# Performance work log

Measured on AMD Instinct MI355X. Metric: run time of the kernel, lower is better.

The kernel has to match this reference:

```python
import jax, jax.numpy as jnp
import numpy as np

K = 3  # number of propagation hops in SGConv


def setup_inputs() -> dict:
    key = jax.random.key(0)
    k1, k2, k3, k4 = jax.random.split(key, 4)
    N, E, F_in, F_out = 100000, 1600000, 32, 64
    x = jax.random.normal(k1, (N, F_in), dtype=jnp.float32)
    edge_index = jax.random.randint(k2, (2, E), 0, N, dtype=jnp.int64)
    # Linear(in_channels, hidden_channels) params, torch layout: W [out, in], b [out]
    lim = 1.0 / np.sqrt(F_in)
    W = jax.random.uniform(k3, (F_out, F_in), minval=-lim, maxval=lim, dtype=jnp.float32)
    b = jax.random.uniform(k4, (F_out,), minval=-lim, maxval=lim, dtype=jnp.float32)
    return {"x": x, "edge_index": edge_index, "W": W, "b": b}


def reference(x, edge_index, W, b):
    N = x.shape[0]
    # gcn_norm: add self-loops with weight 1, symmetric normalization
    loop = jnp.arange(N, dtype=edge_index.dtype)
    src = jnp.concatenate([edge_index[0], loop])  # [E+N] message sources (x_j)
    dst = jnp.concatenate([edge_index[1], loop])  # [E+N] aggregation targets
    ones = jnp.ones(src.shape[0], dtype=x.dtype)
    deg = jax.ops.segment_sum(ones, dst, num_segments=N)  # in-degree incl. self-loop
    dinv = jnp.where(deg > 0, jax.lax.rsqrt(deg), 0.0)
    norm = dinv[src] * dinv[dst]  # [E+N]
    # K hops of normalized sparse propagation: x <- \hat{A} x
    h = x
    for _ in range(K):
        h = jax.ops.segment_sum(norm[:, None] * h[src], dst, num_segments=N)
    # final linear transform
    return h @ W.T + b
```

## Files before the change

### kernel.cpp

```cpp
#include <hip/hip_runtime.h>


#define F_IN 32
#define F_OUT 64
#define SB_SHIFT 13
#define NSB_MAX 16
#define SUB_SHIFT 8
#define SUB (1 << SUB_SHIFT)
#define SPS 32
#define EPB1 2048
#define EPB2 4096
#define SCAP 147456
#define SUBCAP 6144
#define BPS (SCAP / EPB2)

typedef float f4 __attribute__((ext_vector_type(4)));
typedef float f8 __attribute__((ext_vector_type(8)));
typedef _Float16 h4 __attribute__((ext_vector_type(4)));
typedef _Float16 h8 __attribute__((ext_vector_type(8)));
typedef int i2 __attribute__((ext_vector_type(2)));

__global__ __launch_bounds__(256) void k_bin1(const int* __restrict__ ei,
                                              int* __restrict__ scur,
                                              unsigned* __restrict__ b1, int E) {
    __shared__ unsigned stage[EPB1];
    __shared__ unsigned char bidl[EPB1];
    __shared__ int h4w[4][NSB_MAX];
    __shared__ int f4w[4][NSB_MAX];
    __shared__ int lscanx[NSB_MAX], lbase[NSB_MAX];
    unsigned rec[EPB1 / 256];
    int      bk[EPB1 / 256];
    int tid = threadIdx.x;
    int wv = tid >> 6;
    int base = blockIdx.x * EPB1;
    int cnt = E - base; if (cnt > EPB1) cnt = EPB1;

    if (tid < 64) { h4w[tid >> 4][tid & 15] = 0; }
    __syncthreads();
#pragma unroll
    for (int k = 0; k < EPB1 / 256; ++k) {
        int i = base + k * 256 + tid;
        bk[k] = -1;
        if (i < E) {
            unsigned s = (unsigned)ei[i];
            unsigned d = (unsigned)ei[E + i];
            int b = d >> SB_SHIFT;
            rec[k] = (s << SB_SHIFT) | (d & ((1u << SB_SHIFT) - 1));
            bk[k] = b;
            atomicAdd(&h4w[wv][b], 1);
        }
    }
    __syncthreads();
    if (tid < 16) {
        int t0 = h4w[0][tid], t1 = h4w[1][tid], t2 = h4w[2][tid], t3 = h4w[3][tid];
        int tot = t0 + t1 + t2 + t3;
        int inc = tot;
#pragma unroll
        for (int off = 1; off < 16; off <<= 1) {
            int t = __shfl_up(inc, off);
            if (tid >= off) inc += t;
        }
        int excl = inc - tot;
        lscanx[tid] = excl;
        lbase[tid] = tot ? atomicAdd(&scur[tid], tot) : 0;
        f4w[0][tid] = excl;
        f4w[1][tid] = excl + t0;
        f4w[2][tid] = excl + t0 + t1;
        f4w[3][tid] = excl + t0 + t1 + t2;
    }
    __syncthreads();
#pragma unroll
    for (int k = 0; k < EPB1 / 256; ++k) {
        if (bk[k] >= 0) {
            int loc = atomicAdd(&f4w[wv][bk[k]], 1);
            stage[loc] = rec[k];
            bidl[loc] = (unsigned char)bk[k];
        }
    }
    __syncthreads();
    for (int k = 0; k < EPB1 / 256; ++k) {
        int idx = k * 256 + tid;
        if (idx < cnt) {
            int b = bidl[idx];
            b1[(size_t)b * SCAP + lbase[b] + (idx - lscanx[b])] = stage[idx];
        }
    }
}

__global__ __launch_bounds__(256) void k_bin2(const unsigned* __restrict__ b1,
                                              const int* __restrict__ scur,
                                              int* __restrict__ subcur,
                                              unsigned* __restrict__ b2) {
    int sb = blockIdx.x / BPS;
    int base = (blockIdx.x % BPS) * EPB2;
    int count = scur[sb];
    if (base >= count) return;
    int cnt = count - base; if (cnt > EPB2) cnt = EPB2;
    const unsigned* src = b1 + (size_t)sb * SCAP + base;

    __shared__ unsigned stage[EPB2];
    __shared__ unsigned char bidl[EPB2];
    __shared__ int h4w[4][SPS];
    __shared__ int f4w[4][SPS];
    __shared__ int lscanx[SPS], lbase[SPS];
    unsigned rec[EPB2 / 256];
    int tid = threadIdx.x;
    int wv = tid >> 6;
    if (tid < 128) h4w[tid >> 5][tid & 31] = 0;
    __syncthreads();
#pragma unroll
    for (int k = 0; k < EPB2 / 256; ++k) {
        int i = k * 256 + tid;
        rec[k] = 0xFFFFFFFFu;
        if (i < cnt) {
            unsigned r = src[i];
            rec[k] = r;
            atomicAdd(&h4w[wv][(r >> SUB_SHIFT) & (SPS - 1)], 1);
        }
    }
    __syncthreads();
    if (tid < 32) {
        int t0 = h4w[0][tid], t1 = h4w[1][tid], t2 = h4w[2][tid], t3 = h4w[3][tid];
        int tot = t0 + t1 + t2 + t3;
        int inc = tot;
#pragma unroll
        for (int off = 1; off < 32; off <<= 1) {
            int t = __shfl_up(inc, off);
            if (tid >= off) inc += t;
        }
        int excl = inc - tot;
        lscanx[tid] = excl;
        lbase[tid] = tot ? atomicAdd(&subcur[sb * SPS + tid], tot) : 0;
        f4w[0][tid] = excl;
        f4w[1][tid] = excl + t0;
        f4w[2][tid] = excl + t0 + t1;
        f4w[3][tid] = excl + t0 + t1 + t2;
    }
    __syncthreads();
#pragma unroll
    for (int k = 0; k < EPB2 / 256; ++k) {
        if (rec[k] != 0xFFFFFFFFu) {
            int b = (rec[k] >> SUB_SHIFT) & (SPS - 1);
            int loc = atomicAdd(&f4w[wv][b], 1);
            stage[loc] = rec[k];
            bidl[loc] = (unsigned char)b;
        }
    }
    __syncthreads();
    for (int k = 0; k < EPB2 / 256; ++k) {
        int idx = k * 256 + tid;
        if (idx < cnt) {
            unsigned r = stage[idx];
            int b = bidl[idx];
            unsigned packed = ((r >> SB_SHIFT) << SUB_SHIFT) | (r & (SUB - 1));
            b2[(size_t)(sb * SPS + b) * SUBCAP + lbase[b] + (idx - lscanx[b])] = packed;
        }
    }
}

__global__ __launch_bounds__(256) void k_fill3(const unsigned* __restrict__ b2,
                                               const int* __restrict__ subcur,
                                               const f4* __restrict__ x,
                                               float* __restrict__ dinv,
                                               i2* __restrict__ rp2,
                                               int* __restrict__ col,
                                               h8* __restrict__ g0, int N) {
    __shared__ unsigned stage[SUBCAP];
    __shared__ int h[SUB];
    __shared__ float dl[SUB];
    __shared__ int wsum[4];
    int tid = threadIdx.x;
    int g = blockIdx.x;
    int count = subcur[g];
    int sbase = g * SUBCAP;
    int n0 = g << SUB_SHIFT;

    h[tid] = 0;
    for (int e = tid; e < count; e += 256) stage[e] = b2[(size_t)sbase + e];
    __syncthreads();
    for (int e = tid; e < count; e += 256) atomicAdd(&h[stage[e] & (SUB - 1)], 1);
    __syncthreads();

    int deg = h[tid];
    int lane = tid & 63, wid = tid >> 6;
    int inc = deg;
#pragma unroll
    for (int off = 1; off < 64; off <<= 1) {
        int t = __shfl_up(inc, off);
        if (lane >= off) inc += t;
    }
    if (lane == 63) wsum[wid] = inc;
    __syncthreads();
    if (wid == 0) {
        int v = (lane < 4) ? wsum[lane] : 0;
#pragma unroll
        for (int off = 1; off < 4; off <<= 1) {
            int t = __shfl_up(v, off);
            if (lane >= off) v += t;
        }
        if (lane < 4) wsum[lane] = v;
    }
    __syncthreads();
    int incl = inc + (wid ? wsum[wid - 1] : 0);
    int excl = incl - deg;

    int node = n0 + tid;
    float di = rsqrtf(1.0f + (float)deg);
    dl[tid] = di;
    if (node < N) {
        dinv[node] = di;
        rp2[node] = (i2){sbase + excl, sbase + incl};
    }
    h[tid] = excl;
    __syncthreads();

    for (int e = tid; e < count; e += 256) {
        unsigned r = stage[e];
        int slot = sbase + atomicAdd(&h[r & (SUB - 1)], 1);
        col[slot] = (int)(r >> SUB_SHIFT);
    }

    for (int idx = tid; idx < SUB * 4; idx += 256) {
        int nl = idx >> 2;
        int q = idx & 3;
        int node2 = n0 + nl;
        if (node2 < N) {
            int gi = node2 * 8 + q * 2;
            f4 vlo = dl[nl] * x[gi];
            f4 vhi = dl[nl] * x[gi + 1];
            f8 v = __builtin_shufflevector(vlo, vhi, 0, 1, 2, 3, 4, 5, 6, 7);
            g0[(size_t)node2 * 4 + q] = __builtin_convertvector(v, h8);
        }
    }
}

__global__ __launch_bounds__(256) void k_hop_gather(const i2* __restrict__ rp2,
                                                    const int* __restrict__ col,
                                                    const float* __restrict__ dinv,
                                                    const h8* __restrict__ gin,
                                                    h8* __restrict__ gout, int N) {
    int t = blockIdx.x * blockDim.x + threadIdx.x;
    int n = t >> 2;
    if (n >= N) return;
    int q = t & 3;
    i2 r2 = rp2[n];
    int e0 = r2.x, e1 = r2.y;
    f8 a0 = __builtin_convertvector(gin[(size_t)n * 4 + q], f8);
    f8 a1 = {0.f, 0.f, 0.f, 0.f, 0.f, 0.f, 0.f, 0.f};
    int e = e0;
    for (; e + 3 < e1; e += 4) {
        int s0 = col[e], s1 = col[e + 1], s2 = col[e + 2], s3 = col[e + 3];
        h8 h0 = gin[(size_t)s0 * 4 + q];
        h8 h1 = gin[(size_t)s1 * 4 + q];
        h8 h2 = gin[(size_t)s2 * 4 + q];
        h8 h3 = gin[(size_t)s3 * 4 + q];
        a0 += __builtin_convertvector(h0, f8);
        a1 += __builtin_convertvector(h1, f8);
        a0 += __builtin_convertvector(h2, f8);
        a1 += __builtin_convertvector(h3, f8);
    }
    for (; e < e1; ++e) a0 += __builtin_convertvector(gin[(size_t)col[e] * 4 + q], f8);
    float di = dinv[n];
    float sc = di * di;
    f8 r = sc * (a0 + a1);
    gout[(size_t)n * 4 + q] = __builtin_convertvector(r, h8);
}

__global__ __launch_bounds__(256) void k_hop3_linear(const i2* __restrict__ rp2,
                                                     const int* __restrict__ col,
                                                     const float* __restrict__ dinv,
                                                     const h8* __restrict__ gin,
                                                     const float* __restrict__ W,
                                                     const float* __restrict__ bias,
                                                     float* __restrict__ out, int N) {
    __shared__ float Wl[F_OUT][F_IN + 1];
    __shared__ float hl[64][F_IN + 1];
    int tid = threadIdx.x;
    for (int idx = tid; idx < F_OUT * F_IN; idx += 256)
        Wl[idx >> 5][idx & 31] = W[idx];

    int nl = tid >> 2;
    int q = tid & 3;
    int nbase = blockIdx.x * 64;
    int n = nbase + nl;
    if (n < N) {
        i2 r2 = rp2[n];
        int e0 = r2.x, e1 = r2.y;
        f8 a0 = __builtin_convertvector(gin[(size_t)n * 4 + q], f8);
        f8 a1 = {0.f, 0.f, 0.f, 0.f, 0.f, 0.f, 0.f, 0.f};
        int e = e0;
        for (; e + 3 < e1; e += 4) {
            int s0 = col[e], s1 = col[e + 1], s2 = col[e + 2], s3 = col[e + 3];
            h8 h0 = gin[(size_t)s0 * 4 + q];
            h8 h1 = gin[(size_t)s1 * 4 + q];
            h8 h2 = gin[(size_t)s2 * 4 + q];
            h8 h3 = gin[(size_t)s3 * 4 + q];
            a0 += __builtin_convertvector(h0, f8);
            a1 += __builtin_convertvector(h1, f8);
            a0 += __builtin_convertvector(h2, f8);
            a1 += __builtin_convertvector(h3, f8);
        }
        for (; e < e1; ++e) a0 += __builtin_convertvector(gin[(size_t)col[e] * 4 + q], f8);
        float di = dinv[n];
        f8 r = di * (a0 + a1);
#pragma unroll
        for (int i = 0; i < 8; ++i) hl[nl][q * 8 + i] = r[i];
    }
    __syncthreads();
    int o = tid & 63;
    float wreg[F_IN];
#pragma unroll
    for (int f = 0; f < F_IN; ++f) wreg[f] = Wl[o][f];
    float bv = bias[o];
    int nchunk = tid >> 6;
#pragma unroll
    for (int p = 0; p < 16; ++p) {
        int nloc = p * 4 + nchunk;
        int nn = nbase + nloc;
        if (nn < N) {
            float acc = bv;
#pragma unroll
            for (int f = 0; f < F_IN; ++f) acc += hl[nloc][f] * wreg[f];
            out[(size_t)nn * F_OUT + o] = acc;
        }
    }
}

extern "C" void kernel_launch(void* const* d_in, const int* in_sizes, int n_in,
                              void* d_out, int out_size, void* d_ws, size_t ws_size,
                              hipStream_t stream) {
    const float* x  = (const float*)d_in[0];
    const int*   ei = (const int*)d_in[1];
    const float* W  = (const float*)d_in[2];
    const float* b  = (const float*)d_in[3];
    float* out = (float*)d_out;

    const int N = in_sizes[0] / F_IN;
    const int E = in_sizes[1] / 2;
    const int NSB  = (N + (1 << SB_SHIFT) - 1) >> SB_SHIFT;
    const int NSUB = (N + SUB - 1) >> SUB_SHIFT;

    int* scur   = (int*)d_ws;
    int* subcur = scur + NSB_MAX;
    i2*  rp2    = (i2*)(subcur + NSB_MAX * SPS);
    float* dinv = (float*)(rp2 + N);
    unsigned* b1 = (unsigned*)(((uintptr_t)(dinv + N) + 255) & ~(uintptr_t)255);
    unsigned* b2 = b1 + (size_t)NSB_MAX * SCAP;
    int* col     = (int*)(b2 + (size_t)NSB_MAX * SPS * SUBCAP);
    _Float16* hA = (_Float16*)(((uintptr_t)(col + (size_t)NSB_MAX * SPS * SUBCAP) + 255)
                               & ~(uintptr_t)255);
    _Float16* hB = hA + (size_t)N * F_IN;

    const int B = 256;
    dim3 blk(B);

    hipMemsetAsync(scur, 0, (NSB_MAX + NSB_MAX * SPS) * sizeof(int), stream);

    k_bin1<<<dim3((E + EPB1 - 1) / EPB1), blk, 0, stream>>>(ei, scur, b1, E);
    k_bin2<<<dim3(NSB * BPS), blk, 0, stream>>>(b1, scur, subcur, b2);

    k_fill3<<<dim3(NSUB), blk, 0, stream>>>(b2, subcur, (const f4*)x,
                                            dinv, rp2, col, (h8*)hA, N);

    dim3 gHop(((size_t)N * 4 + B - 1) / B);
    k_hop_gather<<<gHop, blk, 0, stream>>>(rp2, col, dinv, (const h8*)hA, (h8*)hB, N);
    k_hop_gather<<<gHop, blk, 0, stream>>>(rp2, col, dinv, (const h8*)hB, (h8*)hA, N);

    k_hop3_linear<<<dim3((N + 63) / 64), blk, 0, stream>>>(rp2, col, dinv,
                                                           (const h8*)hA, W, b, out, N);
}
```

Before: 200.6 us.

## Fuse three propagation hops and linear into one cooperative kernel

Replaces the two per-hop gather launches and the final hop-plus-linear launch with a single cooperative kernel. The hops are separated by grid-wide syncs, and each thread loads its row pointers and degree scale only once. The aim is to remove inter-kernel launch gaps and tail drain between hops. The cost is that all blocks must be resident at once, checked through an occupancy query that assumes 256 compute units, and each grid sync has its own overhead. If the cooperative launch is not possible, the code falls back to the original three launches.

```diff
diff --git a/kernel.cpp b/kernel.cpp
--- a/kernel.cpp
+++ b/kernel.cpp
@@ -1,4 +1,7 @@
 #include <hip/hip_runtime.h>
+#include <hip/hip_cooperative_groups.h>
+
+namespace cg = cooperative_groups;
 
 
 #define F_IN 32
@@ -16,7 +19,6 @@
 
 typedef float f4 __attribute__((ext_vector_type(4)));
 typedef float f8 __attribute__((ext_vector_type(8)));
-typedef _Float16 h4 __attribute__((ext_vector_type(4)));
 typedef _Float16 h8 __attribute__((ext_vector_type(8)));
 typedef int i2 __attribute__((ext_vector_type(2)));
 
@@ -234,17 +236,9 @@
     }
 }
 
-__global__ __launch_bounds__(256) void k_hop_gather(const i2* __restrict__ rp2,
-                                                    const int* __restrict__ col,
-                                                    const float* __restrict__ dinv,
-                                                    const h8* __restrict__ gin,
-                                                    h8* __restrict__ gout, int N) {
-    int t = blockIdx.x * blockDim.x + threadIdx.x;
-    int n = t >> 2;
-    if (n >= N) return;
-    int q = t & 3;
-    i2 r2 = rp2[n];
-    int e0 = r2.x, e1 = r2.y;
+__device__ __forceinline__ f8 gather_row(const h8* __restrict__ gin,
+                                         int e0, int e1, const int* __restrict__ col,
+                                         int n, int q) {
     f8 a0 = __builtin_convertvector(gin[(size_t)n * 4 + q], f8);
     f8 a1 = {0.f, 0.f, 0.f, 0.f, 0.f, 0.f, 0.f, 0.f};
     int e = e0;
@@ -260,10 +254,87 @@
         a1 += __builtin_convertvector(h3, f8);
     }
     for (; e < e1; ++e) a0 += __builtin_convertvector(gin[(size_t)col[e] * 4 + q], f8);
+    return a0 + a1;
+}
+
+__global__ __launch_bounds__(256) void k_hops_fused(const i2* __restrict__ rp2,
+                                                    const int* __restrict__ col,
+                                                    const float* __restrict__ dinv,
+                                                    h8* __restrict__ hA,
+                                                    h8* __restrict__ hB,
+                                                    const float* __restrict__ W,
+                                                    const float* __restrict__ bias,
+                                                    float* __restrict__ out, int N) {
+    cg::grid_group grid = cg::this_grid();
+    __shared__ float Wl[F_OUT][F_IN + 1];
+    __shared__ float hl[64][F_IN + 1];
+    int tid = threadIdx.x;
+    for (int idx = tid; idx < F_OUT * F_IN; idx += 256)
+        Wl[idx >> 5][idx & 31] = W[idx];
+
+    int nl = tid >> 2;
+    int q = tid & 3;
+    int nbase = blockIdx.x * 64;
+    int n = nbase + nl;
+    bool act = n < N;
+    int e0 = 0, e1 = 0;
+    float di = 0.f;
+    if (act) {
+        i2 r2 = rp2[n];
+        e0 = r2.x; e1 = r2.y;
+        di = dinv[n];
+    }
+    float sc = di * di;
+
+    if (act) {
+        f8 acc = gather_row(hA, e0, e1, col, n, q);
+        hB[(size_t)n * 4 + q] = __builtin_convertvector(sc * acc, h8);
+    }
+    grid.sync();
+    if (act) {
+        f8 acc = gather_row(hB, e0, e1, col, n, q);
+        hA[(size_t)n * 4 + q] = __builtin_convertvector(sc * acc, h8);
+    }
+    grid.sync();
+    if (act) {
+        f8 acc = gather_row(hA, e0, e1, col, n, q);
+        f8 r = di * acc;
+#pragma unroll
+        for (int i = 0; i < 8; ++i) hl[nl][q * 8 + i] = r[i];
+    }
+    __syncthreads();
+    int o = tid & 63;
+    float wreg[F_IN];
+#pragma unroll
+    for (int f = 0; f < F_IN; ++f) wreg[f] = Wl[o][f];
+    float bv = bias[o];
+    int nchunk = tid >> 6;
+#pragma unroll
+    for (int p = 0; p < 16; ++p) {
+        int nloc = p * 4 + nchunk;
+        int nn = nbase + nloc;
+        if (nn < N) {
+            float acc = bv;
+#pragma unroll
+            for (int f = 0; f < F_IN; ++f) acc += hl[nloc][f] * wreg[f];
+            out[(size_t)nn * F_OUT + o] = acc;
+        }
+    }
+}
+
+__global__ __launch_bounds__(256) void k_hop_gather(const i2* __restrict__ rp2,
+                                                    const int* __restrict__ col,
+                                                    const float* __restrict__ dinv,
+                                                    const h8* __restrict__ gin,
+                                                    h8* __restrict__ gout, int N) {
+    int t = blockIdx.x * blockDim.x + threadIdx.x;
+    int n = t >> 2;
+    if (n >= N) return;
+    int q = t & 3;
+    i2 r2 = rp2[n];
+    f8 acc = gather_row(gin, r2.x, r2.y, col, n, q);
     float di = dinv[n];
-    float sc = di * di;
-    f8 r = sc * (a0 + a1);
-    gout[(size_t)n * 4 + q] = __builtin_convertvector(r, h8);
+    gout[(size_t)n * 4 + q] = __builtin_convertvector((di * di) * acc, h8);
 }
 
 __global__ __launch_bounds__(256) void k_hop3_linear(const i2* __restrict__ rp2,
@@ -285,24 +356,8 @@
     int n = nbase + nl;
     if (n < N) {
         i2 r2 = rp2[n];
-        int e0 = r2.x, e1 = r2.y;
-        f8 a0 = __builtin_convertvector(gin[(size_t)n * 4 + q], f8);
-        f8 a1 = {0.f, 0.f, 0.f, 0.f, 0.f, 0.f, 0.f, 0.f};
-        int e = e0;
-        for (; e + 3 < e1; e += 4) {
-            int s0 = col[e], s1 = col[e + 1], s2 = col[e + 2], s3 = col[e + 3];
-            h8 h0 = gin[(size_t)s0 * 4 + q];
-            h8 h1 = gin[(size_t)s1 * 4 + q];
-            h8 h2 = gin[(size_t)s2 * 4 + q];
-            h8 h3 = gin[(size_t)s3 * 4 + q];
-            a0 += __builtin_convertvector(h0, f8);
-            a1 += __builtin_convertvector(h1, f8);
-            a0 += __builtin_convertvector(h2, f8);
-            a1 += __builtin_convertvector(h3, f8);
-        }
-        for (; e < e1; ++e) a0 += __builtin_convertvector(gin[(size_t)col[e] * 4 + q], f8);
-        float di = dinv[n];
-        f8 r = di * (a0 + a1);
+        f8 acc = gather_row(gin, r2.x, r2.y, col, n, q);
+        f8 r = dinv[n] * acc;
 #pragma unroll
         for (int i = 0; i < 8; ++i) hl[nl][q * 8 + i] = r[i];
     }
@@ -362,10 +417,30 @@
     k_fill3<<<dim3(NSUB), blk, 0, stream>>>(b2, subcur, (const f4*)x,
                                             dinv, rp2, col, (h8*)hA, N);
 
-    dim3 gHop(((size_t)N * 4 + B - 1) / B);
-    k_hop_gather<<<gHop, blk, 0, stream>>>(rp2, col, dinv, (const h8*)hA, (h8*)hB, N);
-    k_hop_gather<<<gHop, blk, 0, stream>>>(rp2, col, dinv, (const h8*)hB, (h8*)hA, N);
-
-    k_hop3_linear<<<dim3((N + 63) / 64), blk, 0, stream>>>(rp2, col, dinv,
-                                                           (const h8*)hA, W, b, out, N);
-}
+    dim3 gF((N + 63) / 64);
+    int maxb = 0;
+    hipError_t qerr = hipOccupancyMaxActiveBlocksPerMultiprocessor(
+        &maxb, (const void*)k_hops_fused, B, 0);
+    bool coop_ok = (qerr == hipSuccess) && ((long long)maxb * 256 >= (long long)gF.x);
+    if (coop_ok) {
+        const i2* rp2c = rp2;  const int* colc = col;  const float* dinvc = dinv;
+        h8* hA8 = (h8*)hA;     h8* hB8 = (h8*)hB;
+        const float* Wc = W;   const float* bc = b;
+        float* outc = out;     int Nv = N;
+        void* args[] = {(void*)&rp2c, (void*)&colc, (void*)&dinvc,
+                        (void*)&hA8, (void*)&hB8, (void*)&Wc, (void*)&bc,
+                        (void*)&outc, (void*)&Nv};
+        hipError_t lerr = hipLaunchCooperativeKernel((const void*)k_hops_fused,
+                                                     gF, blk, args, 0, stream);
+        if (lerr != hipSuccess) coop_ok = false;
+    }
+    if (!coop_ok) {
+        dim3 gHop(((size_t)N * 4 + B - 1) / B);
+        k_hop_gather<<<gHop, blk, 0, stream>>>(rp2, col, dinv, (const h8*)hA,
+                                               (h8*)hB, N);
+        k_hop_gather<<<gHop, blk, 0, stream>>>(rp2, col, dinv, (const h8*)hB,
+                                               (h8*)hA, N);
+        k_hop3_linear<<<gF, blk, 0, stream>>>(rp2, col, dinv, (const h8*)hA,
+                                              W, b, out, N);
+    }
+}
```

Result: no change. 200.4 us (-0.1%).
